# Optimization experiments

Measured on AMD Instinct MI355X. Metric: run time of the kernel, lower is better.

The kernel has to match this reference:

```python
import jax, jax.numpy as jnp
import numpy as np

N, E = 16384, 524288
IN_C, H1, H2 = 128, 128, 64
EDGE_F = 16
NB = 10                      # binary outputs
MC_GROUPS = (4, 6)           # multi-class group sizes (proto, service)
NC = 10                      # continuous outputs
EPS = 1e-5


def setup_inputs() -> dict:
    key = jax.random.key(0)
    ks = jax.random.split(key, 16)
    def lin(k, fan_in, fan_out):
        s = 1.0 / np.sqrt(fan_in)
        kw, kb = jax.random.split(k)
        return (jax.random.uniform(kw, (fan_in, fan_out), jnp.float32, -s, s),
                jax.random.uniform(kb, (fan_out,), jnp.float32, -s, s))
    w1, b1 = lin(ks[0], IN_C, H1)
    w2, b2 = lin(ks[1], H1, H2)
    w_bin, b_bin = lin(ks[2], H2, NB)
    w_mc, b_mc = lin(ks[3], H2, sum(MC_GROUPS))
    w_cont, b_cont = lin(ks[4], H2, NC)
    w_edge, b_edge = lin(ks[5], 2 * H2, EDGE_F)
    return {
        "x": jax.random.normal(ks[6], (N, IN_C), jnp.float32),
        "edge_index": jax.random.randint(ks[7], (2, E), 0, N, jnp.int64),
        "edge_attr": jax.random.normal(ks[8], (E, EDGE_F), jnp.float32),
        "w1": w1, "b1": b1,
        "bn1_g": jnp.ones((H1,), jnp.float32), "bn1_b": jnp.zeros((H1,), jnp.float32),
        "w2": w2, "b2": b2,
        "bn2_g": jnp.ones((H2,), jnp.float32), "bn2_b": jnp.zeros((H2,), jnp.float32),
        "w_bin": w_bin, "b_bin": b_bin,
        "w_mc": w_mc, "b_mc": b_mc,
        "w_cont": w_cont, "b_cont": b_cont,
        "w_edge": w_edge, "b_edge": b_edge,
    }


def _gcn(x, w, b, src, dst, norm, n):
    # GCNConv: x' = D^-1/2 (A+I) D^-1/2 (x W) + b
    h = x @ w
    msg = h[src] * norm[:, None]
    agg = jax.ops.segment_sum(msg, dst, num_segments=n)
    return agg + b


def _bn(h, g, b):
    m = jnp.mean(h, axis=0)
    v = jnp.var(h, axis=0)
    return g * (h - m) * jax.lax.rsqrt(v + EPS) + b


def reference(x, edge_index, edge_attr, w1, b1, bn1_g, bn1_b, w2, b2, bn2_g, bn2_b,
              w_bin, b_bin, w_mc, b_mc, w_cont, b_cont, w_edge, b_edge):
    n = x.shape[0]
    loops = jnp.arange(n, dtype=edge_index.dtype)
    src = jnp.concatenate([edge_index[0], loops])
    dst = jnp.concatenate([edge_index[1], loops])
    deg = jax.ops.segment_sum(jnp.ones_like(src, dtype=x.dtype), dst, num_segments=n)
    dis = jax.lax.rsqrt(deg)  # deg >= 1 thanks to self-loops
    norm = dis[src] * dis[dst]

    h = jax.nn.relu(_bn(_gcn(x, w1, b1, src, dst, norm, n), bn1_g, bn1_b))
    z = jax.nn.relu(_bn(_gcn(h, w2, b2, src, dst, norm, n), bn2_g, bn2_b))

    # node feature reconstruction: [binary sigmoid | per-group softmax | continuous]
    binary = jax.nn.sigmoid(z @ w_bin + b_bin)
    mc_logits = z @ w_mc + b_mc
    mc_parts, s = [], 0
    for g in MC_GROUPS:
        mc_parts.append(jax.nn.softmax(mc_logits[:, s:s + g], axis=1))
        s += g
    cont = z @ w_cont + b_cont
    reconstructed_x = jnp.concatenate([binary] + mc_parts + [cont], axis=1)

    adj = z @ z.T  # [N, N]

    edge_emb = jnp.concatenate([z[edge_index[0]], z[edge_index[1]]], axis=1)
    edge_features = edge_emb @ w_edge + b_edge
    return (reconstructed_x, adj, edge_features)
```

## Files before the change

### kernel.cpp

```cpp
#include <hip/hip_runtime.h>
#include <hip/hip_bf16.h>
#include <math.h>


constexpr int kN = 16384;
constexpr int kE = 524288;
constexpr float kEps = 1e-5f;

typedef __attribute__((ext_vector_type(8))) short short8v;
typedef __attribute__((ext_vector_type(4))) float f32x4;

__device__ inline float bf2f(unsigned short u) {
  return __uint_as_float(((unsigned)u) << 16);
}
__device__ inline unsigned short f2bf(float f) {
  unsigned u = __float_as_uint(f);
  return (unsigned short)((u + 0x7fff + ((u >> 16) & 1)) >> 16);
}

__global__ void zero_kernel(int* counts, float* sums1, float* sums2,
                            const float* __restrict__ we, __hip_bfloat16* wfr) {
  int i = blockIdx.x * 256 + threadIdx.x;
  if (i < kN) counts[i] = 0;
  if (i < 256) sums1[i] = 0.f;
  if (i < 128) sums2[i] = 0.f;
  if (i < 2048) {
    int f = i >> 9, l = (i >> 3) & 63, j = i & 7;
    int lr = l & 15, lg = l >> 4;
    int krow = f * 32 + lg * 8 + j;
    wfr[i] = __float2bfloat16(we[krow * 16 + lr]);
  }
}

__global__ void hist_kernel(const int* __restrict__ dst, int* __restrict__ counts) {
  int e = blockIdx.x * 256 + threadIdx.x;
  if (e < kE) atomicAdd(&counts[dst[e]], 1);
}

__global__ __launch_bounds__(1024) void scan_kernel(const int* __restrict__ counts,
    int* __restrict__ offsets, int* __restrict__ pos, float* __restrict__ dis) {
  __shared__ int wave_tot[16];
  int tid = threadIdx.x;
  int base = tid * 16;
  int loc[16];
  int s = 0;
#pragma unroll
  for (int i = 0; i < 16; i++) { loc[i] = s; s += counts[base + i]; }
  int lane = tid & 63, wv = tid >> 6;
  int incl = s;
#pragma unroll
  for (int d = 1; d < 64; d <<= 1) {
    int v = __shfl_up(incl, d, 64);
    if (lane >= d) incl += v;
  }
  if (lane == 63) wave_tot[wv] = incl;
  __syncthreads();
  int woff = 0;
  for (int i = 0; i < wv; i++) woff += wave_tot[i];
  int excl = woff + incl - s;
#pragma unroll
  for (int i = 0; i < 16; i++) {
    int o = excl + loc[i];
    offsets[base + i] = o;
    pos[base + i] = o;
    dis[base + i] = rsqrtf((float)counts[base + i] + 1.0f);
  }
}

__global__ void fill_kernel(const int* __restrict__ src, const int* __restrict__ dst,
                            int* __restrict__ pos, int* __restrict__ csr_src) {
  int e = blockIdx.x * 256 + threadIdx.x;
  if (e < kE) {
    int d = dst[e];
    int p = atomicAdd(&pos[d], 1);
    csr_src[p] = src[e];
  }
}

__global__ __launch_bounds__(256) void gemm1_kernel(
    const float* __restrict__ A, const float* __restrict__ W,
    const float* __restrict__ dis, __hip_bfloat16* __restrict__ out) {
  constexpr int BC = 128, NJ = 8, WF4 = 4;
  __shared__ float xs[64 * 33];
  __shared__ float wsh[32 * BC];
  int tid = threadIdx.x;
  int tx = tid & 15, ty = tid >> 4;
  int r0 = blockIdx.x * 64;
  float acc[4][NJ];
#pragma unroll
  for (int r = 0; r < 4; r++)
#pragma unroll
    for (int j = 0; j < NJ; j++) acc[r][j] = 0.f;

  for (int kb = 0; kb < 128; kb += 32) {
    __syncthreads();
#pragma unroll
    for (int q = 0; q < 2; q++) {
      int f = tid + q * 256;
      int row = f >> 3, kq = f & 7;
      float4 v = *(const float4*)(A + (size_t)(r0 + row) * 128 + kb + kq * 4);
      int bb = row * 33 + kq * 4;
      xs[bb + 0] = v.x; xs[bb + 1] = v.y; xs[bb + 2] = v.z; xs[bb + 3] = v.w;
    }
#pragma unroll
    for (int q = 0; q < WF4; q++) {
      int f = tid + q * 256;
      int k = f / (BC / 4), cq = f % (BC / 4);
      *(float4*)&wsh[k * BC + cq * 4] =
          *(const float4*)(W + (size_t)(kb + k) * BC + cq * 4);
    }
    __syncthreads();
#pragma unroll
    for (int kk = 0; kk < 32; kk++) {
      float av[4];
#pragma unroll
      for (int r = 0; r < 4; r++) av[r] = xs[(ty * 4 + r) * 33 + kk];
#pragma unroll
      for (int j = 0; j < NJ; j++) {
        float bv = wsh[kk * BC + tx + j * 16];
#pragma unroll
        for (int r = 0; r < 4; r++) acc[r][j] = fmaf(av[r], bv, acc[r][j]);
      }
    }
  }
#pragma unroll
  for (int r = 0; r < 4; r++) {
    int row = r0 + ty * 4 + r;
    float dr = dis[row];
#pragma unroll
    for (int j = 0; j < NJ; j++)
      out[(size_t)row * BC + tx + j * 16] = __float2bfloat16(acc[r][j] * dr);
  }
}

__global__ __launch_bounds__(256) void gemm2_kernel(
    const unsigned short* __restrict__ A, const float* __restrict__ W,
    const float* __restrict__ sums, const float* __restrict__ g,
    const float* __restrict__ b, const float* __restrict__ dis,
    __hip_bfloat16* __restrict__ out) {
  constexpr int BC = 64, NJ = 4, WF4 = 2;
  __shared__ float xs[64 * 33];
  __shared__ float wsh[32 * BC];
  __shared__ float s_scl[128], s_shf[128];
  int tid = threadIdx.x;
  if (tid < 128) {
    float mean = sums[tid] / (float)kN;
    float var = sums[128 + tid] / (float)kN - mean * mean;
    float inv = rsqrtf(var + kEps);
    float sc = g[tid] * inv;
    s_scl[tid] = sc;
    s_shf[tid] = b[tid] - mean * sc;
  }
  int tx = tid & 15, ty = tid >> 4;
  int r0 = blockIdx.x * 64;
  float acc[4][NJ];
#pragma unroll
  for (int r = 0; r < 4; r++)
#pragma unroll
    for (int j = 0; j < NJ; j++) acc[r][j] = 0.f;

  for (int kb = 0; kb < 128; kb += 32) {
    __syncthreads();
    {
      int row = tid >> 2, kq = tid & 3;
      short8v v8 = *(const short8v*)(A + (size_t)(r0 + row) * 128 + kb + kq * 8);
      int bb = row * 33 + kq * 8;
#pragma unroll
      for (int j = 0; j < 8; j++) {
        int c = kb + kq * 8 + j;
        float v = bf2f((unsigned short)v8[j]);
        xs[bb + j] = fmaxf(0.f, fmaf(v, s_scl[c], s_shf[c]));
      }
    }
#pragma unroll
    for (int q = 0; q < WF4; q++) {
      int f = tid + q * 256;
      int k = f / (BC / 4), cq = f % (BC / 4);
      *(float4*)&wsh[k * BC + cq * 4] =
          *(const float4*)(W + (size_t)(kb + k) * BC + cq * 4);
    }
    __syncthreads();
#pragma unroll
    for (int kk = 0; kk < 32; kk++) {
      float av[4];
#pragma unroll
      for (int r = 0; r < 4; r++) av[r] = xs[(ty * 4 + r) * 33 + kk];
#pragma unroll
      for (int j = 0; j < NJ; j++) {
        float bv = wsh[kk * BC + tx + j * 16];
#pragma unroll
        for (int r = 0; r < 4; r++) acc[r][j] = fmaf(av[r], bv, acc[r][j]);
      }
    }
  }
#pragma unroll
  for (int r = 0; r < 4; r++) {
    int row = r0 + ty * 4 + r;
    float dr = dis[row];
#pragma unroll
    for (int j = 0; j < NJ; j++)
      out[(size_t)row * BC + tx + j * 16] = __float2bfloat16(acc[r][j] * dr);
  }
}

__global__ __launch_bounds__(256) void agg1_kernel(const unsigned short* __restrict__ hs,
    const int* __restrict__ csr_src, const int* __restrict__ offsets,
    const int* __restrict__ counts, const float* __restrict__ dis,
    unsigned short* __restrict__ t1) {
  int tid = threadIdx.x;
  int wv = tid >> 6, lane = tid & 63;
  int d = blockIdx.x * 4 + wv;
  int g = lane >> 4, l = lane & 15;
  float acc[8];
  if (g == 0) {
    short8v v = *(const short8v*)(hs + (size_t)d * 128 + l * 8);
#pragma unroll
    for (int j = 0; j < 8; j++) acc[j] = bf2f((unsigned short)v[j]);
  } else {
#pragma unroll
    for (int j = 0; j < 8; j++) acc[j] = 0.f;
  }
  int s0 = offsets[d], n = counts[d];
  int i = g;
  for (; i + 4 < n; i += 8) {
    int sa = csr_src[s0 + i];
    int sb = csr_src[s0 + i + 4];
    short8v va = *(const short8v*)(hs + (size_t)sa * 128 + l * 8);
    short8v vb = *(const short8v*)(hs + (size_t)sb * 128 + l * 8);
#pragma unroll
    for (int j = 0; j < 8; j++) acc[j] += bf2f((unsigned short)va[j]);
#pragma unroll
    for (int j = 0; j < 8; j++) acc[j] += bf2f((unsigned short)vb[j]);
  }
  if (i < n) {
    int sa = csr_src[s0 + i];
    short8v va = *(const short8v*)(hs + (size_t)sa * 128 + l * 8);
#pragma unroll
    for (int j = 0; j < 8; j++) acc[j] += bf2f((unsigned short)va[j]);
  }
#pragma unroll
  for (int j = 0; j < 8; j++) {
    acc[j] += __shfl_xor(acc[j], 16, 64);
    acc[j] += __shfl_xor(acc[j], 32, 64);
  }
  if (g == 0) {
    float dd = dis[d];
    short8v o;
#pragma unroll
    for (int j = 0; j < 8; j++) o[j] = (short)f2bf(acc[j] * dd);
    *(short8v*)(t1 + (size_t)d * 128 + l * 8) = o;
  }
}

__global__ __launch_bounds__(256) void agg2_kernel(const unsigned short* __restrict__ hs,
    const int* __restrict__ csr_src, const int* __restrict__ offsets,
    const int* __restrict__ counts, const float* __restrict__ dis,
    float* __restrict__ t2) {
  int tid = threadIdx.x;
  int wv = tid >> 6, lane = tid & 63;
  int d = blockIdx.x * 4 + wv;
  int g = lane >> 3, l = lane & 7;
  float acc[8];
  if (g == 0) {
    short8v v = *(const short8v*)(hs + (size_t)d * 64 + l * 8);
#pragma unroll
    for (int j = 0; j < 8; j++) acc[j] = bf2f((unsigned short)v[j]);
  } else {
#pragma unroll
    for (int j = 0; j < 8; j++) acc[j] = 0.f;
  }
  int s0 = offsets[d], n = counts[d];
  int i = g;
  for (; i + 8 < n; i += 16) {
    int sa = csr_src[s0 + i];
    int sb = csr_src[s0 + i + 8];
    short8v va = *(const short8v*)(hs + (size_t)sa * 64 + l * 8);
    short8v vb = *(const short8v*)(hs + (size_t)sb * 64 + l * 8);
#pragma unroll
    for (int j = 0; j < 8; j++) acc[j] += bf2f((unsigned short)va[j]);
#pragma unroll
    for (int j = 0; j < 8; j++) acc[j] += bf2f((unsigned short)vb[j]);
  }
  if (i < n) {
    int sa = csr_src[s0 + i];
    short8v va = *(const short8v*)(hs + (size_t)sa * 64 + l * 8);
#pragma unroll
    for (int j = 0; j < 8; j++) acc[j] += bf2f((unsigned short)va[j]);
  }
#pragma unroll
  for (int j = 0; j < 8; j++) {
    acc[j] += __shfl_xor(acc[j], 8, 64);
    acc[j] += __shfl_xor(acc[j], 16, 64);
    acc[j] += __shfl_xor(acc[j], 32, 64);
  }
  if (g == 0) {
    float dd = dis[d];
    float* o = t2 + (size_t)d * 64 + l * 8;
    f32x4 o0 = {acc[0] * dd, acc[1] * dd, acc[2] * dd, acc[3] * dd};
    f32x4 o1 = {acc[4] * dd, acc[5] * dd, acc[6] * dd, acc[7] * dd};
    *(f32x4*)o = o0;
    *(f32x4*)(o + 4) = o1;
  }
}

template <int C, bool BF16>
__global__ __launch_bounds__(256) void stats_kernel(const void* __restrict__ t,
                                                    float* __restrict__ sums) {
  constexpr int RP = 256 / C;
  int c = threadIdx.x % C;
  int rr = threadIdx.x / C;
  float s = 0.f, s2 = 0.f;
  for (int r = blockIdx.x * RP + rr; r < kN; r += gridDim.x * RP) {
    float v;
    if constexpr (BF16) v = bf2f(((const unsigned short*)t)[(size_t)r * C + c]);
    else v = ((const float*)t)[(size_t)r * C + c];
    s += v;
    s2 += v * v;
  }
  atomicAdd(&sums[c], s);
  atomicAdd(&sums[C + c], s2);
}

__global__ __launch_bounds__(256) void zheads_kernel(const float* __restrict__ t2,
    const float* __restrict__ sums, const float* __restrict__ gg,
    const float* __restrict__ bb2,
    const float* __restrict__ wbin, const float* __restrict__ bbin,
    const float* __restrict__ wmc, const float* __restrict__ bmc,
    const float* __restrict__ wcont, const float* __restrict__ bcont,
    float* __restrict__ out0, unsigned short* __restrict__ zb) {
  __shared__ float wT[30 * 64];
  __shared__ float bias[32];
  __shared__ float s_scl[64], s_shf[64];
  int tid = threadIdx.x;
  for (int idx = tid; idx < 1920; idx += 256) {
    int j = idx >> 6, k = idx & 63;
    const float* src = (j < 10) ? wbin : (j < 20) ? wmc : wcont;
    wT[idx] = src[k * 10 + (j % 10)];
  }
  if (tid < 30)
    bias[tid] = (tid < 10) ? bbin[tid] : (tid < 20) ? bmc[tid - 10] : bcont[tid - 20];
  if (tid < 64) {
    float mean = sums[tid] / (float)kN;
    float var = sums[64 + tid] / (float)kN - mean * mean;
    float inv = rsqrtf(var + kEps);
    float sc = gg[tid] * inv;
    s_scl[tid] = sc;
    s_shf[tid] = bb2[tid] - mean * sc;
  }
  __syncthreads();
  int n = blockIdx.x * 256 + tid;
  float zr[64];
  const float4* t4 = (const float4*)(t2 + (size_t)n * 64);
#pragma unroll
  for (int q = 0; q < 16; q++) {
    float4 v = t4[q];
    zr[4 * q + 0] = fmaxf(0.f, fmaf(v.x, s_scl[4 * q + 0], s_shf[4 * q + 0]));
    zr[4 * q + 1] = fmaxf(0.f, fmaf(v.y, s_scl[4 * q + 1], s_shf[4 * q + 1]));
    zr[4 * q + 2] = fmaxf(0.f, fmaf(v.z, s_scl[4 * q + 2], s_shf[4 * q + 2]));
    zr[4 * q + 3] = fmaxf(0.f, fmaf(v.w, s_scl[4 * q + 3], s_shf[4 * q + 3]));
  }
  unsigned short* zrow = zb + (size_t)n * 64;
#pragma unroll
  for (int q = 0; q < 8; q++) {
    short8v o;
#pragma unroll
    for (int j = 0; j < 8; j++) o[j] = (short)f2bf(zr[q * 8 + j]);
    *(short8v*)(zrow + q * 8) = o;
  }
  float acc[30];
#pragma unroll
  for (int j = 0; j < 30; j++) {
    float s = bias[j];
#pragma unroll
    for (int kc = 0; kc < 16; kc++) {
      f32x4 wv = *(const f32x4*)&wT[j * 64 + kc * 4];
      s = fmaf(zr[4 * kc + 0], wv.x, s);
      s = fmaf(zr[4 * kc + 1], wv.y, s);
      s = fmaf(zr[4 * kc + 2], wv.z, s);
      s = fmaf(zr[4 * kc + 3], wv.w, s);
    }
    acc[j] = s;
  }
  float* o = out0 + (size_t)n * 30;
#pragma unroll
  for (int j = 0; j < 10; j++) o[j] = 1.f / (1.f + expf(-acc[j]));
  float m1 = fmaxf(fmaxf(acc[10], acc[11]), fmaxf(acc[12], acc[13]));
  float e1[4], s1 = 0.f;
#pragma unroll
  for (int j = 0; j < 4; j++) { e1[j] = expf(acc[10 + j] - m1); s1 += e1[j]; }
#pragma unroll
  for (int j = 0; j < 4; j++) o[10 + j] = e1[j] / s1;
  float m2 = acc[14];
#pragma unroll
  for (int j = 15; j < 20; j++) m2 = fmaxf(m2, acc[j]);
  float e2[6], s2 = 0.f;
#pragma unroll
  for (int j = 0; j < 6; j++) { e2[j] = expf(acc[14 + j] - m2); s2 += e2[j]; }
#pragma unroll
  for (int j = 0; j < 6; j++) o[14 + j] = e2[j] / s2;
#pragma unroll
  for (int j = 0; j < 10; j++) o[20 + j] = acc[20 + j];
}

__global__ __launch_bounds__(256) void adjedge_kernel(const short* __restrict__ zb,
    const int* __restrict__ srcs, const int* __restrict__ dsts,
    const short* __restrict__ wfr, const float* __restrict__ be,
    float* __restrict__ adj, float* __restrict__ eout) {
  __shared__ float cs[128 * 132];
  int tid = threadIdx.x;
  int wid = tid >> 6, lane = tid & 63;
  int lr = lane & 15, lg = lane >> 4;

  if (blockIdx.x < 1024) {
    float* es = &cs[wid * 256];
    int gw = blockIdx.x * 4 + wid;
    short8v bfr[4];
#pragma unroll
    for (int f = 0; f < 4; f++)
      bfr[f] = *(const short8v*)(wfr + ((size_t)f * 64 + lane) * 8);
    float bias = be[lr];
    for (int t = 0; t < 8; t++) {
      int e0 = (gw * 8 + t) * 16;
      int se = srcs[e0 + lr], de = dsts[e0 + lr];
      short8v a0 = *(const short8v*)(zb + (size_t)se * 64 + lg * 8);
      short8v a1 = *(const short8v*)(zb + (size_t)se * 64 + 32 + lg * 8);
      short8v a2 = *(const short8v*)(zb + (size_t)de * 64 + lg * 8);
      short8v a3 = *(const short8v*)(zb + (size_t)de * 64 + 32 + lg * 8);
      f32x4 acc = {0.f, 0.f, 0.f, 0.f};
      acc = __builtin_amdgcn_mfma_f32_16x16x32_bf16(a0, bfr[0], acc, 0, 0, 0);
      acc = __builtin_amdgcn_mfma_f32_16x16x32_bf16(a1, bfr[1], acc, 0, 0, 0);
      acc = __builtin_amdgcn_mfma_f32_16x16x32_bf16(a2, bfr[2], acc, 0, 0, 0);
      acc = __builtin_amdgcn_mfma_f32_16x16x32_bf16(a3, bfr[3], acc, 0, 0, 0);
#pragma unroll
      for (int r = 0; r < 4; r++)
        es[(lg * 4 + r) * 16 + lr] = acc[r] + bias;
      f32x4 v = *(const f32x4*)&es[lane * 4];
      *(f32x4*)(eout + (size_t)e0 * 16 + lane * 4) = v;
    }
    return;
  }

  int bid = blockIdx.x - 1024;
  int bcol = bid & 127;
  int brow = bid >> 7;
  int li0 = (wid >> 1) * 64;
  int lj0 = (wid & 1) * 64;
  int i0 = brow * 128 + li0;
  int j0 = bcol * 128 + lj0;
  short8v a[4][2], b[4][2];
#pragma unroll
  for (int mt = 0; mt < 4; mt++)
#pragma unroll
    for (int ks = 0; ks < 2; ks++)
      a[mt][ks] = *(const short8v*)(zb + (size_t)(i0 + mt * 16 + lr) * 64 + ks * 32 + lg * 8);
#pragma unroll
  for (int nt = 0; nt < 4; nt++)
#pragma unroll
    for (int ks = 0; ks < 2; ks++)
      b[nt][ks] = *(const short8v*)(zb + (size_t)(j0 + nt * 16 + lr) * 64 + ks * 32 + lg * 8);
  f32x4 acc[4][4];
#pragma unroll
  for (int mt = 0; mt < 4; mt++)
#pragma unroll
    for (int nt = 0; nt < 4; nt++) {
      f32x4 zz = {0.f, 0.f, 0.f, 0.f};
      acc[mt][nt] = zz;
    }
#pragma unroll
  for (int ks = 0; ks < 2; ks++)
#pragma unroll
    for (int mt = 0; mt < 4; mt++)
#pragma unroll
      for (int nt = 0; nt < 4; nt++)
        acc[mt][nt] = __builtin_amdgcn_mfma_f32_16x16x32_bf16(a[mt][ks], b[nt][ks],
                                                              acc[mt][nt], 0, 0, 0);
#pragma unroll
  for (int mt = 0; mt < 4; mt++)
#pragma unroll
    for (int nt = 0; nt < 4; nt++)
#pragma unroll
      for (int r = 0; r < 4; r++)
        cs[(li0 + mt * 16 + lg * 4 + r) * 132 + lj0 + nt * 16 + lr] = acc[mt][nt][r];
  __syncthreads();
  int row = tid >> 5;
  int c4 = tid & 31;
  size_t gbase = (size_t)(brow * 128 + row) * kN + bcol * 128 + c4 * 4;
  const float* lbase = &cs[row * 132 + c4 * 4];
#pragma unroll
  for (int it = 0; it < 16; it++) {
    f32x4 v = *(const f32x4*)(lbase + it * 8 * 132);
    *(f32x4*)(adj + gbase + (size_t)it * 8 * kN) = v;
  }
}

extern "C" void kernel_launch(void* const* d_in, const int* in_sizes, int n_in,
                              void* d_out, int out_size, void* d_ws, size_t ws_size,
                              hipStream_t stream) {
  const float* x      = (const float*)d_in[0];
  const int*   ei     = (const int*)d_in[1];
  const float* w1     = (const float*)d_in[3];
  const float* bn1_g  = (const float*)d_in[5];
  const float* bn1_b  = (const float*)d_in[6];
  const float* w2     = (const float*)d_in[7];
  const float* bn2_g  = (const float*)d_in[9];
  const float* bn2_b  = (const float*)d_in[10];
  const float* w_bin  = (const float*)d_in[11];
  const float* b_bin  = (const float*)d_in[12];
  const float* w_mc   = (const float*)d_in[13];
  const float* b_mc   = (const float*)d_in[14];
  const float* w_cont = (const float*)d_in[15];
  const float* b_cont = (const float*)d_in[16];
  const float* w_edge = (const float*)d_in[17];
  const float* b_edge = (const float*)d_in[18];

  float* out0 = (float*)d_out;
  float* adj  = out0 + (size_t)kN * 30;
  float* eout = adj + (size_t)kN * kN;

  char* wp = (char*)d_ws;
  auto alloc = [&](size_t bytes) {
    char* p = wp;
    wp += (bytes + 255) & ~(size_t)255;
    return p;
  };
  int*   counts  = (int*)alloc((size_t)kN * 4);
  int*   offsets = (int*)alloc((size_t)kN * 4);
  int*   pos     = (int*)alloc((size_t)kN * 4);
  int*   csr_src = (int*)alloc((size_t)kE * 4);
  float* dis     = (float*)alloc((size_t)kN * 4);
  float* sums1   = (float*)alloc(256 * 4);
  float* sums2   = (float*)alloc(128 * 4);
  unsigned short* hs1 = (unsigned short*)alloc((size_t)kN * 128 * 2);
  unsigned short* t1  = (unsigned short*)alloc((size_t)kN * 128 * 2);
  unsigned short* hs2 = (unsigned short*)alloc((size_t)kN * 64 * 2);
  float* t2      = (float*)alloc((size_t)kN * 64 * 4);
  unsigned short* zb  = (unsigned short*)alloc((size_t)kN * 64 * 2);
  __hip_bfloat16* wfr = (__hip_bfloat16*)alloc(2048 * 2);

  const int* esrc = ei;
  const int* edst = ei + kE;

  zero_kernel<<<dim3(64), dim3(256), 0, stream>>>(counts, sums1, sums2, w_edge, wfr);
  hist_kernel<<<dim3(2048), dim3(256), 0, stream>>>(edst, counts);
  scan_kernel<<<dim3(1), dim3(1024), 0, stream>>>(counts, offsets, pos, dis);
  fill_kernel<<<dim3(2048), dim3(256), 0, stream>>>(esrc, edst, pos, csr_src);

  gemm1_kernel<<<dim3(kN / 64), dim3(256), 0, stream>>>(
      x, w1, dis, (__hip_bfloat16*)hs1);
  agg1_kernel<<<dim3(kN / 4), dim3(256), 0, stream>>>(
      hs1, csr_src, offsets, counts, dis, t1);
  stats_kernel<128, true><<<dim3(256), dim3(256), 0, stream>>>(t1, sums1);

  gemm2_kernel<<<dim3(kN / 64), dim3(256), 0, stream>>>(
      t1, w2, sums1, bn1_g, bn1_b, dis, (__hip_bfloat16*)hs2);
  agg2_kernel<<<dim3(kN / 4), dim3(256), 0, stream>>>(
      hs2, csr_src, offsets, counts, dis, t2);
  stats_kernel<64, false><<<dim3(256), dim3(256), 0, stream>>>(t2, sums2);

  zheads_kernel<<<dim3(kN / 256), dim3(256), 0, stream>>>(
      t2, sums2, bn2_g, bn2_b, w_bin, b_bin, w_mc, b_mc, w_cont, b_cont, out0, zb);

  adjedge_kernel<<<dim3(1024 + 16384), dim3(256), 0, stream>>>(
      (const short*)zb, esrc, edst, (const short*)wfr, b_edge, adj, eout);
}
```

Before: 422.3 us.

## Fuse degree histogram with first GEMM, move source normalization into aggregation

The first GEMM no longer depends on the degree normalization, so it is merged into the histogram launch as extra blocks. This removes one kernel launch and lets the GEMM overlap with the atomic histogram. In exchange, the per-source dis scaling is now applied inside agg1 with an extra gather of dis per edge plus an FMA per element. The self-loop term is also scaled by dis[d] before the final scaling, which preserves the original math.

Result: no change. 419.7 us (-0.6%).

```diff
diff --git a/kernel.cpp b/kernel.cpp
--- a/kernel.cpp
+++ b/kernel.cpp
@@ -32,9 +32,65 @@
   }
 }
 
-__global__ void hist_kernel(const int* __restrict__ dst, int* __restrict__ counts) {
-  int e = blockIdx.x * 256 + threadIdx.x;
-  if (e < kE) atomicAdd(&counts[dst[e]], 1);
+__global__ __launch_bounds__(256) void histgemm1_kernel(
+    const int* __restrict__ dst, int* __restrict__ counts,
+    const float* __restrict__ A, const float* __restrict__ W,
+    __hip_bfloat16* __restrict__ out) {
+  if (blockIdx.x < 2048) {
+    int e = blockIdx.x * 256 + threadIdx.x;
+    atomicAdd(&counts[dst[e]], 1);
+    return;
+  }
+  constexpr int BC = 128, NJ = 8, WF4 = 4;
+  __shared__ float xs[64 * 33];
+  __shared__ float wsh[32 * BC];
+  int tid = threadIdx.x;
+  int tx = tid & 15, ty = tid >> 4;
+  int r0 = (blockIdx.x - 2048) * 64;
+  float acc[4][NJ];
+#pragma unroll
+  for (int r = 0; r < 4; r++)
+#pragma unroll
+    for (int j = 0; j < NJ; j++) acc[r][j] = 0.f;
+
+  for (int kb = 0; kb < 128; kb += 32) {
+    __syncthreads();
+#pragma unroll
+    for (int q = 0; q < 2; q++) {
+      int f = tid + q * 256;
+      int row = f >> 3, kq = f & 7;
+      float4 v = *(const float4*)(A + (size_t)(r0 + row) * 128 + kb + kq * 4);
+      int bb = row * 33 + kq * 4;
+      xs[bb + 0] = v.x; xs[bb + 1] = v.y; xs[bb + 2] = v.z; xs[bb + 3] = v.w;
+    }
+#pragma unroll
+    for (int q = 0; q < WF4; q++) {
+      int f = tid + q * 256;
+      int k = f / (BC / 4), cq = f % (BC / 4);
+      *(float4*)&wsh[k * BC + cq * 4] =
+          *(const float4*)(W + (size_t)(kb + k) * BC + cq * 4);
+    }
+    __syncthreads();
+#pragma unroll
+    for (int kk = 0; kk < 32; kk++) {
+      float av[4];
+#pragma unroll
+      for (int r = 0; r < 4; r++) av[r] = xs[(ty * 4 + r) * 33 + kk];
+#pragma unroll
+      for (int j = 0; j < NJ; j++) {
+        float bv = wsh[kk * BC + tx + j * 16];
+#pragma unroll
+        for (int r = 0; r < 4; r++) acc[r][j] = fmaf(av[r], bv, acc[r][j]);
+      }
+    }
+  }
+#pragma unroll
+  for (int r = 0; r < 4; r++) {
+    int row = r0 + ty * 4 + r;
+#pragma unroll
+    for (int j = 0; j < NJ; j++)
+      out[(size_t)row * BC + tx + j * 16] = __float2bfloat16(acc[r][j]);
+  }
 }
 
 __global__ __launch_bounds__(1024) void scan_kernel(const int* __restrict__ counts,
@@ -74,62 +130,6 @@
     int d = dst[e];
     int p = atomicAdd(&pos[d], 1);
     csr_src[p] = src[e];
-  }
-}
-
-__global__ __launch_bounds__(256) void gemm1_kernel(
-    const float* __restrict__ A, const float* __restrict__ W,
-    const float* __restrict__ dis, __hip_bfloat16* __restrict__ out) {
-  constexpr int BC = 128, NJ = 8, WF4 = 4;
-  __shared__ float xs[64 * 33];
-  __shared__ float wsh[32 * BC];
-  int tid = threadIdx.x;
-  int tx = tid & 15, ty = tid >> 4;
-  int r0 = blockIdx.x * 64;
-  float acc[4][NJ];
-#pragma unroll
-  for (int r = 0; r < 4; r++)
-#pragma unroll
-    for (int j = 0; j < NJ; j++) acc[r][j] = 0.f;
-
-  for (int kb = 0; kb < 128; kb += 32) {
-    __syncthreads();
-#pragma unroll
-    for (int q = 0; q < 2; q++) {
-      int f = tid + q * 256;
-      int row = f >> 3, kq = f & 7;
-      float4 v = *(const float4*)(A + (size_t)(r0 + row) * 128 + kb + kq * 4);
-      int bb = row * 33 + kq * 4;
-      xs[bb + 0] = v.x; xs[bb + 1] = v.y; xs[bb + 2] = v.z; xs[bb + 3] = v.w;
-    }
-#pragma unroll
-    for (int q = 0; q < WF4; q++) {
-      int f = tid + q * 256;
-      int k = f / (BC / 4), cq = f % (BC / 4);
-      *(float4*)&wsh[k * BC + cq * 4] =
-          *(const float4*)(W + (size_t)(kb + k) * BC + cq * 4);
-    }
-    __syncthreads();
-#pragma unroll
-    for (int kk = 0; kk < 32; kk++) {
-      float av[4];
-#pragma unroll
-      for (int r = 0; r < 4; r++) av[r] = xs[(ty * 4 + r) * 33 + kk];
-#pragma unroll
-      for (int j = 0; j < NJ; j++) {
-        float bv = wsh[kk * BC + tx + j * 16];
-#pragma unroll
-        for (int r = 0; r < 4; r++) acc[r][j] = fmaf(av[r], bv, acc[r][j]);
-      }
-    }
-  }
-#pragma unroll
-  for (int r = 0; r < 4; r++) {
-    int row = r0 + ty * 4 + r;
-    float dr = dis[row];
-#pragma unroll
-    for (int j = 0; j < NJ; j++)
-      out[(size_t)row * BC + tx + j * 16] = __float2bfloat16(acc[r][j] * dr);
   }
 }
 
@@ -211,11 +211,12 @@
   int wv = tid >> 6, lane = tid & 63;
   int d = blockIdx.x * 4 + wv;
   int g = lane >> 4, l = lane & 15;
+  float dd = dis[d];
   float acc[8];
   if (g == 0) {
     short8v v = *(const short8v*)(hs + (size_t)d * 128 + l * 8);
 #pragma unroll
-    for (int j = 0; j < 8; j++) acc[j] = bf2f((unsigned short)v[j]);
+    for (int j = 0; j < 8; j++) acc[j] = bf2f((unsigned short)v[j]) * dd;
   } else {
 #pragma unroll
     for (int j = 0; j < 8; j++) acc[j] = 0.f;
@@ -225,18 +226,20 @@
   for (; i + 4 < n; i += 8) {
     int sa = csr_src[s0 + i];
     int sb = csr_src[s0 + i + 4];
+    float da = dis[sa], db = dis[sb];
     short8v va = *(const short8v*)(hs + (size_t)sa * 128 + l * 8);
     short8v vb = *(const short8v*)(hs + (size_t)sb * 128 + l * 8);
 #pragma unroll
-    for (int j = 0; j < 8; j++) acc[j] += bf2f((unsigned short)va[j]);
-#pragma unroll
-    for (int j = 0; j < 8; j++) acc[j] += bf2f((unsigned short)vb[j]);
+    for (int j = 0; j < 8; j++) acc[j] = fmaf(bf2f((unsigned short)va[j]), da, acc[j]);
+#pragma unroll
+    for (int j = 0; j < 8; j++) acc[j] = fmaf(bf2f((unsigned short)vb[j]), db, acc[j]);
   }
   if (i < n) {
     int sa = csr_src[s0 + i];
+    float da = dis[sa];
     short8v va = *(const short8v*)(hs + (size_t)sa * 128 + l * 8);
 #pragma unroll
-    for (int j = 0; j < 8; j++) acc[j] += bf2f((unsigned short)va[j]);
+    for (int j = 0; j < 8; j++) acc[j] = fmaf(bf2f((unsigned short)va[j]), da, acc[j]);
   }
 #pragma unroll
   for (int j = 0; j < 8; j++) {
@@ -244,7 +247,6 @@
     acc[j] += __shfl_xor(acc[j], 32, 64);
   }
   if (g == 0) {
-    float dd = dis[d];
     short8v o;
 #pragma unroll
     for (int j = 0; j < 8; j++) o[j] = (short)f2bf(acc[j] * dd);
@@ -541,12 +543,11 @@
   const int* edst = ei + kE;
 
   zero_kernel<<<dim3(64), dim3(256), 0, stream>>>(counts, sums1, sums2, w_edge, wfr);
-  hist_kernel<<<dim3(2048), dim3(256), 0, stream>>>(edst, counts);
+  histgemm1_kernel<<<dim3(2048 + 256), dim3(256), 0, stream>>>(
+      edst, counts, x, w1, (__hip_bfloat16*)hs1);
   scan_kernel<<<dim3(1), dim3(1024), 0, stream>>>(counts, offsets, pos, dis);
   fill_kernel<<<dim3(2048), dim3(256), 0, stream>>>(esrc, edst, pos, csr_src);
 
-  gemm1_kernel<<<dim3(kN / 64), dim3(256), 0, stream>>>(
-      x, w1, dis, (__hip_bfloat16*)hs1);
   agg1_kernel<<<dim3(kN / 4), dim3(256), 0, stream>>>(
       hs1, csr_src, offsets, counts, dis, t1);
   stats_kernel<128, true><<<dim3(256), dim3(256), 0, stream>>>(t1, sums1);
```
